# Kernel tuning notes

Measured on AMD Instinct MI355X. Metric: run time of the kernel, lower is better.

The kernel has to match this reference:

```python
import jax, jax.numpy as jnp
import numpy as np

B, T, D, H, KH, HD, F, L, V = 2, 2048, 1024, 16, 4, 64, 4096, 4, 32000
G = H // KH  # num_key_value_groups
EPS = 1e-6
SCALE = HD ** -0.5


def setup_inputs() -> dict:
    key = jax.random.key(0)
    ks = jax.random.split(key, 8)
    std = 0.02
    return {
        "input_ids": jax.random.randint(ks[0], (B, T), 0, V, dtype=jnp.int32),
        "embed_w": jax.random.normal(ks[1], (V, D), jnp.float32) * std,
        "pos_w": jax.random.normal(ks[2], (T, D), jnp.float32) * std,
        "ln1_w": jnp.ones((L, D), jnp.float32),
        "ln2_w": jnp.ones((L, D), jnp.float32),
        "wq": jax.random.normal(ks[3], (L, D, H * HD), jnp.float32) * std,
        "wkv": jax.random.normal(ks[4], (L, D, 2 * KH * HD), jnp.float32) * std,
        "wo": jax.random.normal(ks[5], (L, H * HD, D), jnp.float32) * std,
        "w1": jax.random.normal(ks[6], (L, D, F), jnp.float32) * std,
        "w2": jax.random.normal(ks[7], (L, F, D), jnp.float32) * std,
        "norm_w": jnp.ones((D,), jnp.float32),
    }


def _rmsnorm(x, w):
    return x * jax.lax.rsqrt(jnp.mean(x * x, axis=-1, keepdims=True) + EPS) * w


def reference(input_ids, embed_w, pos_w, ln1_w, ln2_w, wq, wkv, wo, w1, w2, norm_w):
    causal = jnp.tril(jnp.ones((T, T), dtype=bool))  # True = keep
    x = embed_w[input_ids] + pos_w[:T]  # [B,T,D]
    for l in range(L):
        h = _rmsnorm(x, ln1_w[l])
        q = (h @ wq[l]).reshape(B, T, H, HD)
        kv = h @ wkv[l]
        k, v = jnp.split(kv, 2, axis=-1)
        k = jnp.repeat(k.reshape(B, T, KH, HD), G, axis=2)  # GQA repeat_interleave
        v = jnp.repeat(v.reshape(B, T, KH, HD), G, axis=2)
        scores = jnp.einsum("bqhd,bkhd->bhqk", q, k) * SCALE
        scores = jnp.where(causal, scores, -jnp.inf)
        p = jax.nn.softmax(scores, axis=-1)
        o = jnp.einsum("bhqk,bkhd->bqhd", p, v).reshape(B, T, H * HD)
        x = x + o @ wo[l]
        h = _rmsnorm(x, ln2_w[l])
        x = x + jax.nn.gelu(h @ w1[l], approximate=False) @ w2[l]
    x = _rmsnorm(x, norm_w)
    logits = x @ embed_w.T  # tied lm_head
    return logits
```

## Files before the change

kernel.cpp:

```cpp
#include <hip/hip_runtime.h>
#include <hip/hip_bf16.h>

#define DI __device__ __forceinline__

typedef unsigned short u16;
typedef unsigned int u32;
typedef __attribute__((ext_vector_type(8))) short bf16x8;
typedef __attribute__((ext_vector_type(4))) short bf16x4;
typedef __attribute__((ext_vector_type(4))) float f32x4;

#define B_   2
#define T_   2048
#define D_   1024
#define H_   16
#define KH_  4
#define HD_  64
#define F_   4096
#define L_   4
#define V_   32000
#define M_   (B_ * T_)
#define QKVN (H_*HD_ + 2*KH_*HD_)

DI u16 f2bf(float f) {
  __hip_bfloat16 h = __float2bfloat16(f);
  return *reinterpret_cast<u16*>(&h);
}

DI float bf2f(u16 b) {
  __hip_bfloat16 h = *reinterpret_cast<__hip_bfloat16*>(&b);
  return __bfloat162float(h);
}

DI void gl_lds16(const void* g, void* l) {
  __builtin_amdgcn_global_load_lds(
      (const __attribute__((address_space(1))) u32*)g,
      (__attribute__((address_space(3))) u32*)l, 16, 0, 0);
}

#define BARRIER() do { asm volatile("" ::: "memory"); __builtin_amdgcn_s_barrier(); asm volatile("" ::: "memory"); } while (0)
#define LGK0()    asm volatile("s_waitcnt lgkmcnt(0)" ::: "memory")
#define VMC(n)    asm volatile("s_waitcnt vmcnt(" #n ")" ::: "memory")
#define PRIO(p)   __builtin_amdgcn_s_setprio(p)

__global__ __launch_bounds__(256) void embed_kernel(const int* __restrict__ ids,
                                                    const float* __restrict__ ew,
                                                    const float* __restrict__ pw,
                                                    float* __restrict__ x) {
  const int row = blockIdx.x;
  const int t = row & (T_ - 1);
  const int id = ids[row];
  float4 e = reinterpret_cast<const float4*>(ew + (size_t)id * D_)[threadIdx.x];
  float4 p = reinterpret_cast<const float4*>(pw + (size_t)t * D_)[threadIdx.x];
  e.x += p.x; e.y += p.y; e.z += p.z; e.w += p.w;
  reinterpret_cast<float4*>(x + (size_t)row * D_)[threadIdx.x] = e;
}

__global__ __launch_bounds__(256) void conv_kernel(const float* __restrict__ W,
                                                   u16* __restrict__ Wb) {
  const size_t i = (size_t)blockIdx.x * 256 + threadIdx.x;
  float4 v = reinterpret_cast<const float4*>(W)[i];
  ushort4 ov;
  ov.x = f2bf(v.x); ov.y = f2bf(v.y); ov.z = f2bf(v.z); ov.w = f2bf(v.w);
  reinterpret_cast<ushort4*>(Wb)[i] = ov;
}

__global__ __launch_bounds__(256) void convt_fused(const float* __restrict__ wq,
                                                   const float* __restrict__ wkv,
                                                   const float* __restrict__ wo,
                                                   const float* __restrict__ w1,
                                                   const float* __restrict__ w2,
                                                   u16* __restrict__ wtq,
                                                   u16* __restrict__ wto,
                                                   u16* __restrict__ wt1,
                                                   u16* __restrict__ wt2) {
  const int t = blockIdx.x;
  const float* W; u16* Wt; int K, N, local;
  if (t < 1024)      { W = wq;  Wt = wtq;               K = 1024; N = 1024; local = t; }
  else if (t < 1536) { W = wkv; Wt = wtq + 1024*1024;   K = 1024; N = 512;  local = t - 1024; }
  else if (t < 2560) { W = wo;  Wt = wto;               K = 1024; N = 1024; local = t - 1536; }
  else if (t < 6656) { W = w1;  Wt = wt1;               K = 1024; N = 4096; local = t - 2560; }
  else               { W = w2;  Wt = wt2;               K = 4096; N = 1024; local = t - 6656; }
  const int nk = K >> 5;
  const int k0 = (local % nk) * 32, n0 = (local / nk) * 32;
  __shared__ float tb[32][33];
  const int tx = threadIdx.x & 31, ty = threadIdx.x >> 5;
  #pragma unroll
  for (int i = 0; i < 4; i++)
    tb[ty + i*8][tx] = W[(size_t)(k0 + ty + i*8) * N + n0 + tx];
  __syncthreads();
  #pragma unroll
  for (int i = 0; i < 4; i++)
    Wt[(size_t)(n0 + ty + i*8) * K + k0 + tx] = f2bf(tb[tx][ty + i*8]);
}

__global__ __launch_bounds__(256) void rmsnorm_kernel(const float* __restrict__ x,
                                                      const float* __restrict__ w,
                                                      u16* __restrict__ out) {
  const int row = blockIdx.x;
  const int tid = threadIdx.x;
  float4 v = reinterpret_cast<const float4*>(x + (size_t)row * D_)[tid];
  float ss = v.x*v.x + v.y*v.y + v.z*v.z + v.w*v.w;
  #pragma unroll
  for (int off = 32; off > 0; off >>= 1) ss += __shfl_down(ss, off, 64);
  __shared__ float red[4];
  if ((tid & 63) == 0) red[tid >> 6] = ss;
  __syncthreads();
  const float tot = red[0] + red[1] + red[2] + red[3];
  const float rstd = rsqrtf(tot * (1.0f / D_) + 1e-6f);
  float4 wv = reinterpret_cast<const float4*>(w)[tid];
  ushort4 ov;
  ov.x = f2bf(v.x * rstd * wv.x);
  ov.y = f2bf(v.y * rstd * wv.y);
  ov.z = f2bf(v.z * rstd * wv.z);
  ov.w = f2bf(v.w * rstd * wv.w);
  reinterpret_cast<ushort4*>(out + (size_t)row * D_)[tid] = ov;
}

template <int EPI>
__global__ __launch_bounds__(256) void gemm_bt(const u16* __restrict__ A,
                                               const u16* __restrict__ Bt,
                                               const float* __restrict__ res,
                                               u16* __restrict__ Cb,
                                               float* __restrict__ Cf,
                                               int M, int N, int K) {
  __shared__ u16 As[128 * 64];
  __shared__ u16 Bs[128 * 64];
  const int tid = threadIdx.x;
  const int nx = N >> 7;
  const int nwg = nx * (M >> 7);
  const int cpx = nwg >> 3;
  const int bid = blockIdx.x;
  const int wg = (bid & 7) * cpx + (bid >> 3);
  const int n0 = (wg % nx) << 7;
  const int m0 = (wg / nx) << 7;
  const int lane = tid & 63, wave = tid >> 6;
  const int wm = wave >> 1, wn = wave & 1;
  const int l15 = lane & 15, l4 = lane >> 4;
  const int srow = tid >> 3, scol = (tid & 7) * 8;
  const u16* ag = A + (size_t)(m0 + srow) * K + scol;
  const u16* bg = Bt + (size_t)(n0 + srow) * K + scol;
  u16* asd = &As[srow * 64 + scol];
  u16* bsd = &Bs[srow * 64 + scol];
  f32x4 acc[4][4] = {};
  const int nk = K >> 6;
  for (int kt = 0; kt < nk; kt++) {
    const int k0 = kt * 64;
    __syncthreads();
    #pragma unroll
    for (int i = 0; i < 4; i++) gl_lds16(ag + (size_t)i*32*K + k0, asd + i*32*64);
    #pragma unroll
    for (int i = 0; i < 4; i++) gl_lds16(bg + (size_t)i*32*K + k0, bsd + i*32*64);
    __syncthreads();
    #pragma unroll
    for (int s = 0; s < 2; s++) {
      bf16x8 af[4], bfv[4];
      #pragma unroll
      for (int i = 0; i < 4; i++)
        af[i] = *reinterpret_cast<const bf16x8*>(&As[(wm*64 + i*16 + l15)*64 + s*32 + l4*8]);
      #pragma unroll
      for (int j = 0; j < 4; j++)
        bfv[j] = *reinterpret_cast<const bf16x8*>(&Bs[(wn*64 + j*16 + l15)*64 + s*32 + l4*8]);
      #pragma unroll
      for (int i = 0; i < 4; i++)
        #pragma unroll
        for (int j = 0; j < 4; j++)
          acc[i][j] = __builtin_amdgcn_mfma_f32_16x16x32_bf16(bfv[j], af[i], acc[i][j], 0, 0, 0);
    }
  }
  #pragma unroll
  for (int i = 0; i < 4; i++) {
    const int row = m0 + wm*64 + i*16 + l15;
    #pragma unroll
    for (int j = 0; j < 4; j++) {
      const int colb = n0 + wn*64 + j*16 + l4*4;
      const size_t idx = (size_t)row * N + colb;
      const f32x4 v = acc[i][j];
      if (EPI == 0) {
        ushort4 ov;
        ov.x = f2bf(v[0]); ov.y = f2bf(v[1]); ov.z = f2bf(v[2]); ov.w = f2bf(v[3]);
        *reinterpret_cast<ushort4*>(&Cb[idx]) = ov;
      } else {
        const float4 rv = *reinterpret_cast<const float4*>(&res[idx]);
        float4 ov;
        ov.x = v[0] + rv.x; ov.y = v[1] + rv.y; ov.z = v[2] + rv.z; ov.w = v[3] + rv.w;
        *reinterpret_cast<float4*>(&Cf[idx]) = ov;
      }
    }
  }
}

template <int EPI>
__global__ __launch_bounds__(512, 2) void gemm256(const u16* __restrict__ A,
                                                  const u16* __restrict__ Bt,
                                                  u16* __restrict__ Cb,
                                                  float* __restrict__ Cf,
                                                  int M, int N, int K) {
  __shared__ char lds[131072];
  char* const AsB = lds;
  char* const BsB = lds + 65536;
  const int tid = threadIdx.x;
  const int lane = tid & 63, wave = tid >> 6;
  const int wm = wave >> 2, wn = wave & 3;
  const int l15 = lane & 15, l4 = lane >> 4;

  const int nm = M >> 8;
  const int nwg = nm * (N >> 8);
  const int cpx = nwg >> 3;
  const int bid = blockIdx.x;
  const int wg = (bid & 7) * cpx + (bid >> 3);
  const int m0 = (wg % nm) << 8;
  const int n0 = (wg / nm) << 8;

  const u16* const Atile = A + (size_t)m0 * K;
  const u16* const Btile = Bt + (size_t)n0 * K;

  int soff[2][2], pd[2][2];
  #pragma unroll
  for (int h = 0; h < 2; ++h)
    #pragma unroll
    for (int jj = 0; jj < 2; ++jj) {
      const int row = h*128 + jj*64 + (tid >> 3);
      const int sl  = (tid & 7) ^ (row & 7);
      soff[h][jj] = row * K + sl * 8;
      pd[h][jj]   = h*16384 + jj*8192 + tid*16;
    }
  const int swz = (l15 & 7) << 4;
  const int rb0 = l15*128 + ((l4*16)      ^ swz);
  const int rb1 = l15*128 + ((64 + l4*16) ^ swz);

  #define STA(S,H,T) do { const u16* g_ = Atile + (T)*64; char* d_ = AsB + (S)*32768; \
      gl_lds16(g_ + soff[H][0], d_ + pd[H][0]); gl_lds16(g_ + soff[H][1], d_ + pd[H][1]); } while (0)
  #define STB(S,H,T) do { const u16* g_ = Btile + (T)*64; char* d_ = BsB + (S)*32768; \
      gl_lds16(g_ + soff[H][0], d_ + pd[H][0]); gl_lds16(g_ + soff[H][1], d_ + pd[H][1]); } while (0)
  #define RDA(S,GI,RB) (*reinterpret_cast<const bf16x8*>(AsB + (S)*32768 + (GI)*2048 + (RB)))
  #define RDB(S,GJ,RB) (*reinterpret_cast<const bf16x8*>(BsB + (S)*32768 + (GJ)*2048 + (RB)))

  f32x4 acc[8][4] = {};
  bf16x8 Ar[4][2], Br[4][2];

  #define RDA03(S) { _Pragma("unroll") for (int i=0;i<4;++i){ Ar[i][0]=RDA(S,i*2+wm,rb0); Ar[i][1]=RDA(S,i*2+wm,rb1);} }
  #define RDA47(S) { _Pragma("unroll") for (int i=0;i<4;++i){ Ar[i][0]=RDA(S,(i+4)*2+wm,rb0); Ar[i][1]=RDA(S,(i+4)*2+wm,rb1);} }
  #define RDB01(S) { _Pragma("unroll") for (int j=0;j<2;++j){ Br[j][0]=RDB(S,j*4+wn,rb0); Br[j][1]=RDB(S,j*4+wn,rb1);} }
  #define RDB23(S) { _Pragma("unroll") for (int j=2;j<4;++j){ Br[j][0]=RDB(S,j*4+wn,rb0); Br[j][1]=RDB(S,j*4+wn,rb1);} }
  #define MFQ(IO,JL) { _Pragma("unroll") for (int i=0;i<4;++i) _Pragma("unroll") for (int jj=0;jj<2;++jj) { \
      acc[(IO)+i][(JL)+jj] = __builtin_amdgcn_mfma_f32_16x16x32_bf16(Br[(JL)+jj][0], Ar[i][0], acc[(IO)+i][(JL)+jj],0,0,0); \
      acc[(IO)+i][(JL)+jj] = __builtin_amdgcn_mfma_f32_16x16x32_bf16(Br[(JL)+jj][1], Ar[i][1], acc[(IO)+i][(JL)+jj],0,0,0); } }

  STA(0,0,0); STA(0,1,0); STB(0,0,0); STB(0,1,0);
  VMC(4);
  STA(1,0,1); STB(1,0,1); STB(1,1,1);
  VMC(6);
  BARRIER();

  const int niter = K >> 7;
  for (int it = 0; it < niter; ++it) {
    const int t0 = it*2, t1 = t0 + 1;
    const bool pf = (it + 1 < niter);
    RDA03(0); RDB01(0); STA(1,1,t1);
    BARRIER(); LGK0(); PRIO(1); MFQ(0,0); PRIO(0); BARRIER();
    RDB23(0); if (pf) STA(0,0,t0+2);
    BARRIER(); LGK0(); PRIO(1); MFQ(0,2); PRIO(0); BARRIER();
    RDA47(0); if (pf) STB(0,0,t0+2);
    BARRIER(); LGK0(); PRIO(1); MFQ(4,0); PRIO(0); BARRIER();
    if (pf) { STB(0,1,t0+2); VMC(6); } else { VMC(0); }
    BARRIER(); PRIO(1); MFQ(4,2); PRIO(0); BARRIER();
    RDA03(1); RDB01(1); if (pf) STA(0,1,t0+2);
    BARRIER(); LGK0(); PRIO(1); MFQ(0,0); PRIO(0); BARRIER();
    RDB23(1); if (pf) STA(1,0,t1+2);
    BARRIER(); LGK0(); PRIO(1); MFQ(0,2); PRIO(0); BARRIER();
    RDA47(1); if (pf) STB(1,0,t1+2);
    BARRIER(); LGK0(); PRIO(1); MFQ(4,0); PRIO(0); BARRIER();
    if (pf) { STB(1,1,t1+2); VMC(6); }
    BARRIER(); PRIO(1); MFQ(4,2); PRIO(0); BARRIER();
  }

  #pragma unroll
  for (int i = 0; i < 8; ++i) {
    const int row = m0 + (i*2 + wm)*16 + l15;
    #pragma unroll
    for (int j = 0; j < 4; ++j) {
      const int colb = n0 + (j*4 + wn)*16 + l4*4;
      const f32x4 v = acc[i][j];
      if (EPI == 0) {
        *reinterpret_cast<f32x4*>(&Cf[(size_t)row * N + colb]) = v;
      } else {
        ushort4 ov;
        #pragma unroll
        for (int rr = 0; rr < 4; ++rr) {
          const float g = 0.5f * v[rr] * (1.0f + erff(v[rr] * 0.70710678118f));
          ((u16*)&ov)[rr] = f2bf(g);
        }
        *reinterpret_cast<ushort4*>(&Cb[(size_t)row * N + colb]) = ov;
      }
    }
  }
  #undef STA
  #undef STB
  #undef RDA
  #undef RDB
  #undef RDA03
  #undef RDA47
  #undef RDB01
  #undef RDB23
  #undef MFQ
}

__global__ __launch_bounds__(512) void attn_kernel(const u16* __restrict__ qkv,
                                                   u16* __restrict__ o) {
  const int qtA = blockIdx.x;
  const int qtB = 15 - qtA;
  const int h  = blockIdx.y;
  const int b  = blockIdx.z;
  const int kh = h / (H_ / KH_);
  __shared__ u16 Ks[2][64 * 64];
  __shared__ u16 Vt[2][64 * 66];
  __shared__ u16 Pl[16][16 * 68];
  const int tid = threadIdx.x, lane = tid & 63, wave = tid >> 6;
  const int l15 = lane & 15, l4 = lane >> 4;
  const size_t Mrow = (size_t)b * T_;

  bf16x8 qfA[2], qfB[2];
  {
    const u16* qpA = qkv + (Mrow + qtA*128 + wave*16 + l15) * QKVN + h*HD_ + l4*8;
    const u16* qpB = qkv + (Mrow + qtB*128 + wave*16 + l15) * QKVN + h*HD_ + l4*8;
    qfA[0] = *reinterpret_cast<const bf16x8*>(qpA);
    qfA[1] = *reinterpret_cast<const bf16x8*>(qpA + 32);
    qfB[0] = *reinterpret_cast<const bf16x8*>(qpB);
    qfB[1] = *reinterpret_cast<const bf16x8*>(qpB + 32);
    #pragma unroll
    for (int s = 0; s < 2; s++)
      #pragma unroll
      for (int j = 0; j < 8; j++) {
        qfA[s][j] = (short)f2bf(bf2f((u16)qfA[s][j]) * 0.18033688f);
        qfB[s][j] = (short)f2bf(bf2f((u16)qfB[s][j]) * 0.18033688f);
      }
  }
  float mA = -1e30f, lA = 0.0f, mB = -1e30f, lB = 0.0f;
  f32x4 oaccA[4] = {}, oaccB[4] = {};

  const int srow = tid >> 3, scol = (tid & 7) * 8;
  const int vp = (tid >> 4) * 2;
  const int vd = (tid & 15) * 4;
  const u16* const kbase = qkv + Mrow * QKVN + D_ + kh*HD_;
  const u16* const vbase = kbase + KH_*HD_;

  {
    gl_lds16(kbase + (size_t)srow * QKVN + scol, &Ks[0][srow*64 + scol]);
    const u16* vg = vbase + (size_t)vp * QKVN + vd;
    bf16x4 v0 = *reinterpret_cast<const bf16x4*>(vg);
    bf16x4 v1 = *reinterpret_cast<const bf16x4*>(vg + QKVN);
    #pragma unroll
    for (int j = 0; j < 4; j++) {
      const u32 pk = (u32)(u16)v0[j] | ((u32)(u16)v1[j] << 16);
      *reinterpret_cast<u32*>(&Vt[0][(vd + j)*66 + vp]) = pk;
    }
  }
  __syncthreads();

  const int nktA = 2*qtA + 2;
  const int nktB = 2*qtB + 2;
  for (int kt = 0; kt < nktB; kt++) {
    const int cur = kt & 1;
    const bool pf = kt + 1 < nktB;
    bf16x4 v0n, v1n;
    if (pf) {
      gl_lds16(kbase + (size_t)((kt+1)*64 + srow) * QKVN + scol,
               &Ks[1-cur][srow*64 + scol]);
      const u16* vg = vbase + (size_t)((kt+1)*64 + vp) * QKVN + vd;
      v0n = *reinterpret_cast<const bf16x4*>(vg);
      v1n = *reinterpret_cast<const bf16x4*>(vg + QKVN);
    }

    f32x4 saB[4] = {};
    #pragma unroll
    for (int s = 0; s < 2; s++)
      #pragma unroll
      for (int n = 0; n < 4; n++) {
        bf16x8 kf = *reinterpret_cast<const bf16x8*>(&Ks[cur][(n*16 + l15)*64 + s*32 + l4*8]);
        saB[n] = __builtin_amdgcn_mfma_f32_16x16x32_bf16(kf, qfB[s], saB[n], 0, 0, 0);
      }
    if (kt >= 2*qtB) {
      const int qloc = wave*16 + l15;
      const int kb = kt*64 - qtB*128 + l4*4;
      #pragma unroll
      for (int n = 0; n < 4; n++)
        #pragma unroll
        for (int r = 0; r < 4; r++)
          if (kb + n*16 + r > qloc) saB[n][r] = -1e30f;
    }
    {
      float mx;
      {
        f32x4 m4;
        #pragma unroll
        for (int r = 0; r < 4; r++)
          m4[r] = fmaxf(fmaxf(saB[0][r], saB[1][r]), fmaxf(saB[2][r], saB[3][r]));
        mx = fmaxf(fmaxf(m4[0], m4[1]), fmaxf(m4[2], m4[3]));
        mx = fmaxf(mx, __shfl_xor(mx, 16, 64));
        mx = fmaxf(mx, __shfl_xor(mx, 32, 64));
      }
      if (__any((int)(mx - mB > 8.0f))) {
        const float nm = fmaxf(mB, mx);
        const float alpha = exp2f(mB - nm);
        mB = nm; lB *= alpha;
        #pragma unroll
        for (int r = 0; r < 4; r++) {
          const float a_r = __shfl(alpha, l4*4 + r, 64);
          #pragma unroll
          for (int n = 0; n < 4; n++) oaccB[n][r] *= a_r;
        }
      }
      float rs = 0.0f;
      u16* pw = &Pl[8 + wave][0];
      #pragma unroll
      for (int n = 0; n < 4; n++) {
        ushort4 pv;
        #pragma unroll
        for (int r = 0; r < 4; r++) {
          const float p = exp2f(saB[n][r] - mB);
          rs += p;
          ((u16*)&pv)[r] = f2bf(p);
        }
        *reinterpret_cast<ushort4*>(&pw[l15*68 + n*16 + l4*4]) = pv;
      }
      rs += __shfl_xor(rs, 16, 64);
      rs += __shfl_xor(rs, 32, 64);
      lB += rs;
    }

    if (pf) {
      #pragma unroll
      for (int j = 0; j < 4; j++) {
        const u32 pk = (u32)(u16)v0n[j] | ((u32)(u16)v1n[j] << 16);
        *reinterpret_cast<u32*>(&Vt[1-cur][(vd + j)*66 + vp]) = pk;
      }
    }

    asm volatile("s_waitcnt lgkmcnt(0)" ::: "memory");
    #pragma unroll
    for (int s = 0; s < 2; s++) {
      bf16x8 pa = *reinterpret_cast<const bf16x8*>(&Pl[8 + wave][l15*68 + s*32 + l4*8]);
      #pragma unroll
      for (int n = 0; n < 4; n++) {
        bf16x8 vb = *reinterpret_cast<const bf16x8*>(&Vt[cur][(n*16 + l15)*66 + s*32 + l4*8]);
        oaccB[n] = __builtin_amdgcn_mfma_f32_16x16x32_bf16(pa, vb, oaccB[n], 0, 0, 0);
      }
    }

    if (kt < nktA) {
      f32x4 sa[4] = {};
      #pragma unroll
      for (int s = 0; s < 2; s++)
        #pragma unroll
        for (int n = 0; n < 4; n++) {
          bf16x8 kf = *reinterpret_cast<const bf16x8*>(&Ks[cur][(n*16 + l15)*64 + s*32 + l4*8]);
          sa[n] = __builtin_amdgcn_mfma_f32_16x16x32_bf16(kf, qfA[s], sa[n], 0, 0, 0);
        }
      if (kt >= 2*qtA) {
        const int qloc = wave*16 + l15;
        const int kb = kt*64 - qtA*128 + l4*4;
        #pragma unroll
        for (int n = 0; n < 4; n++)
          #pragma unroll
          for (int r = 0; r < 4; r++)
            if (kb + n*16 + r > qloc) sa[n][r] = -1e30f;
      }
      float mx;
      {
        f32x4 m4;
        #pragma unroll
        for (int r = 0; r < 4; r++)
          m4[r] = fmaxf(fmaxf(sa[0][r], sa[1][r]), fmaxf(sa[2][r], sa[3][r]));
        mx = fmaxf(fmaxf(m4[0], m4[1]), fmaxf(m4[2], m4[3]));
        mx = fmaxf(mx, __shfl_xor(mx, 16, 64));
        mx = fmaxf(mx, __shfl_xor(mx, 32, 64));
      }
      if (__any((int)(mx - mA > 8.0f))) {
        const float nm = fmaxf(mA, mx);
        const float alpha = exp2f(mA - nm);
        mA = nm; lA *= alpha;
        #pragma unroll
        for (int r = 0; r < 4; r++) {
          const float a_r = __shfl(alpha, l4*4 + r, 64);
          #pragma unroll
          for (int n = 0; n < 4; n++) oaccA[n][r] *= a_r;
        }
      }
      float rs = 0.0f;
      u16* pw = &Pl[wave][0];
      #pragma unroll
      for (int n = 0; n < 4; n++) {
        ushort4 pv;
        #pragma unroll
        for (int r = 0; r < 4; r++) {
          const float p = exp2f(sa[n][r] - mA);
          rs += p;
          ((u16*)&pv)[r] = f2bf(p);
        }
        *reinterpret_cast<ushort4*>(&pw[l15*68 + n*16 + l4*4]) = pv;
      }
      rs += __shfl_xor(rs, 16, 64);
      rs += __shfl_xor(rs, 32, 64);
      lA += rs;
      asm volatile("s_waitcnt lgkmcnt(0)" ::: "memory");
      #pragma unroll
      for (int s = 0; s < 2; s++) {
        bf16x8 pa = *reinterpret_cast<const bf16x8*>(&pw[l15*68 + s*32 + l4*8]);
        #pragma unroll
        for (int n = 0; n < 4; n++) {
          bf16x8 vb = *reinterpret_cast<const bf16x8*>(&Vt[cur][(n*16 + l15)*66 + s*32 + l4*8]);
          oaccA[n] = __builtin_amdgcn_mfma_f32_16x16x32_bf16(pa, vb, oaccA[n], 0, 0, 0);
        }
      }
    }

    __syncthreads();
  }
  {
    float lr[4];
    #pragma unroll
    for (int r = 0; r < 4; r++) lr[r] = __shfl(lA, l4*4 + r, 64);
    #pragma unroll
    for (int n = 0; n < 4; n++)
      #pragma unroll
      for (int r = 0; r < 4; r++) {
        const float ov = oaccA[n][r] / lr[r];
        const size_t row = Mrow + qtA*128 + wave*16 + l4*4 + r;
        o[row * (size_t)(H_*HD_) + h*HD_ + n*16 + l15] = f2bf(ov);
      }
    #pragma unroll
    for (int r = 0; r < 4; r++) lr[r] = __shfl(lB, l4*4 + r, 64);
    #pragma unroll
    for (int n = 0; n < 4; n++)
      #pragma unroll
      for (int r = 0; r < 4; r++) {
        const float ov = oaccB[n][r] / lr[r];
        const size_t row = Mrow + qtB*128 + wave*16 + l4*4 + r;
        o[row * (size_t)(H_*HD_) + h*HD_ + n*16 + l15] = f2bf(ov);
      }
  }
}

#define OFF_X     0ull
#define OFF_H     16777216ull
#define OFF_QKV   25165824ull
#define OFF_O     37748736ull
#define OFF_U     46137344ull
#define OFF_WTQ   79691776ull
#define OFF_WTO   82837504ull
#define OFF_WT1   84934656ull
#define OFF_WT2   93323264ull
#define OFF_EBF   101711872ull

extern "C" void kernel_launch(void* const* d_in, const int* in_sizes, int n_in,
                              void* d_out, int out_size, void* d_ws, size_t ws_size,
                              hipStream_t stream) {
  const int*   ids = (const int*)  d_in[0];
  const float* ew  = (const float*)d_in[1];
  const float* pw  = (const float*)d_in[2];
  const float* ln1 = (const float*)d_in[3];
  const float* ln2 = (const float*)d_in[4];
  const float* wq  = (const float*)d_in[5];
  const float* wkv = (const float*)d_in[6];
  const float* wo  = (const float*)d_in[7];
  const float* w1  = (const float*)d_in[8];
  const float* w2  = (const float*)d_in[9];
  const float* nw  = (const float*)d_in[10];
  float* out = (float*)d_out;

  char* ws = (char*)d_ws;
  float* x   = (float*)(ws + OFF_X);
  u16*   h   = (u16*)  (ws + OFF_H);
  u16*   qkv = (u16*)  (ws + OFF_QKV);
  u16*   o   = (u16*)  (ws + OFF_O);
  u16*   u   = (u16*)  (ws + OFF_U);
  u16*   wtq = (u16*)  (ws + OFF_WTQ);
  u16*   wto = (u16*)  (ws + OFF_WTO);
  u16*   wt1 = (u16*)  (ws + OFF_WT1);
  u16*   wt2 = (u16*)  (ws + OFF_WT2);
  u16*   ebf = (u16*)  (ws + OFF_EBF);

  embed_kernel<<<M_, 256, 0, stream>>>(ids, ew, pw, x);
  conv_kernel<<<(V_*D_/4)/256, 256, 0, stream>>>(ew, ebf);

  for (int l = 0; l < L_; l++) {
    convt_fused<<<10752, 256, 0, stream>>>(
        wq  + (size_t)l*D_*(H_*HD_),
        wkv + (size_t)l*D_*(2*KH_*HD_),
        wo  + (size_t)l*(H_*HD_)*D_,
        w1  + (size_t)l*D_*F_,
        w2  + (size_t)l*F_*D_,
        wtq, wto, wt1, wt2);

    rmsnorm_kernel<<<M_, 256, 0, stream>>>(x, ln1 + (size_t)l*D_, h);
    gemm_bt<0><<<(QKVN/128)*(M_/128), 256, 0, stream>>>(h, wtq, nullptr, qkv, nullptr, M_, QKVN, D_);
    attn_kernel<<<dim3(T_/256, H_, B_), 512, 0, stream>>>(qkv, o);
    gemm_bt<1><<<(D_/128)*(M_/128), 256, 0, stream>>>(o, wto, x, nullptr, x, M_, D_, H_*HD_);
    rmsnorm_kernel<<<M_, 256, 0, stream>>>(x, ln2 + (size_t)l*D_, h);
    gemm256<1><<<dim3((F_/256)*(M_/256)), 512, 0, stream>>>(h, wt1, u, nullptr, M_, F_, D_);
    gemm_bt<1><<<(D_/128)*(M_/128), 256, 0, stream>>>(u, wt2, x, nullptr, x, M_, D_, F_);
  }

  rmsnorm_kernel<<<M_, 256, 0, stream>>>(x, nw, h);
  gemm256<0><<<dim3((V_/256)*(M_/256)), 512, 0, stream>>>(h, ebf, nullptr, out, M_, V_, D_);
}
```

Baseline: 1.475 ms.

## Make 256-tile GEMM persistent and prefetch next tile during current tile's tail

Converts the 256x256 GEMM into a persistent kernel launched with 256 workgroups, each looping over output tiles with a stride of 256. During the last K-step of the current tile it issues the global-to-LDS loads for the next tile's first K-slices, so that load latency overlaps the final MFMAs and the epilogue. K is hardcoded to 1024. The code assumes consecutive tiles of a workgroup share the same A rows, which holds because the tile stride is a multiple of the 16 M-tiles. The FFN up-projection has exactly 256 tiles, so it gains little; the main target is the LM-head GEMM.

Result: no change. 1.499 ms (+1.7%).

```diff
diff --git a/kernel.cpp b/kernel.cpp
--- a/kernel.cpp
+++ b/kernel.cpp
@@ -190,11 +190,12 @@
 }
 
 template <int EPI>
-__global__ __launch_bounds__(512, 2) void gemm256(const u16* __restrict__ A,
-                                                  const u16* __restrict__ Bt,
-                                                  u16* __restrict__ Cb,
-                                                  float* __restrict__ Cf,
-                                                  int M, int N, int K) {
+__global__ __launch_bounds__(512, 2) void gemm256p(const u16* __restrict__ A,
+                                                   const u16* __restrict__ Bt,
+                                                   u16* __restrict__ Cb,
+                                                   float* __restrict__ Cf,
+                                                   int M, int N) {
+  const int K = 1024;
   __shared__ char lds[131072];
   char* const AsB = lds;
   char* const BsB = lds + 65536;
@@ -204,15 +205,9 @@
   const int l15 = lane & 15, l4 = lane >> 4;
 
   const int nm = M >> 8;
-  const int nwg = nm * (N >> 8);
-  const int cpx = nwg >> 3;
+  const int nt_all = nm * (N >> 8);
   const int bid = blockIdx.x;
-  const int wg = (bid & 7) * cpx + (bid >> 3);
-  const int m0 = (wg % nm) << 8;
-  const int n0 = (wg / nm) << 8;
-
-  const u16* const Atile = A + (size_t)m0 * K;
-  const u16* const Btile = Bt + (size_t)n0 * K;
+  const int wg0 = (bid & 7) * 32 + (bid >> 3);
 
   int soff[2][2], pd[2][2];
   #pragma unroll
@@ -228,9 +223,9 @@
   const int rb0 = l15*128 + ((l4*16)      ^ swz);
   const int rb1 = l15*128 + ((64 + l4*16) ^ swz);
 
-  #define STA(S,H,T) do { const u16* g_ = Atile + (T)*64; char* d_ = AsB + (S)*32768; \
+  #define STA(P,S,H,T) do { const u16* g_ = (P) + (T)*64; char* d_ = AsB + (S)*32768; \
       gl_lds16(g_ + soff[H][0], d_ + pd[H][0]); gl_lds16(g_ + soff[H][1], d_ + pd[H][1]); } while (0)
-  #define STB(S,H,T) do { const u16* g_ = Btile + (T)*64; char* d_ = BsB + (S)*32768; \
+  #define STB(P,S,H,T) do { const u16* g_ = (P) + (T)*64; char* d_ = BsB + (S)*32768; \
       gl_lds16(g_ + soff[H][0], d_ + pd[H][0]); gl_lds16(g_ + soff[H][1], d_ + pd[H][1]); } while (0)
   #define RDA(S,GI,RB) (*reinterpret_cast<const bf16x8*>(AsB + (S)*32768 + (GI)*2048 + (RB)))
   #define RDB(S,GJ,RB) (*reinterpret_cast<const bf16x8*>(BsB + (S)*32768 + (GJ)*2048 + (RB)))
@@ -246,53 +241,84 @@
       acc[(IO)+i][(JL)+jj] = __builtin_amdgcn_mfma_f32_16x16x32_bf16(Br[(JL)+jj][0], Ar[i][0], acc[(IO)+i][(JL)+jj],0,0,0); \
       acc[(IO)+i][(JL)+jj] = __builtin_amdgcn_mfma_f32_16x16x32_bf16(Br[(JL)+jj][1], Ar[i][1], acc[(IO)+i][(JL)+jj],0,0,0); } }
 
-  STA(0,0,0); STA(0,1,0); STB(0,0,0); STB(0,1,0);
+  int tt = wg0;
+  const u16* Ac = A + (size_t)((tt % nm) << 8) * K;
+  const u16* Bc = Bt + (size_t)((tt / nm) << 8) * K;
+
+  STA(Ac,0,0,0); STA(Ac,0,1,0); STB(Bc,0,0,0); STB(Bc,0,1,0);
   VMC(4);
-  STA(1,0,1); STB(1,0,1); STB(1,1,1);
+  STA(Ac,1,0,1); STB(Bc,1,0,1); STB(Bc,1,1,1);
   VMC(6);
   BARRIER();
 
-  const int niter = K >> 7;
-  for (int it = 0; it < niter; ++it) {
-    const int t0 = it*2, t1 = t0 + 1;
-    const bool pf = (it + 1 < niter);
-    RDA03(0); RDB01(0); STA(1,1,t1);
-    BARRIER(); LGK0(); PRIO(1); MFQ(0,0); PRIO(0); BARRIER();
-    RDB23(0); if (pf) STA(0,0,t0+2);
-    BARRIER(); LGK0(); PRIO(1); MFQ(0,2); PRIO(0); BARRIER();
-    RDA47(0); if (pf) STB(0,0,t0+2);
-    BARRIER(); LGK0(); PRIO(1); MFQ(4,0); PRIO(0); BARRIER();
-    if (pf) { STB(0,1,t0+2); VMC(6); } else { VMC(0); }
-    BARRIER(); PRIO(1); MFQ(4,2); PRIO(0); BARRIER();
-    RDA03(1); RDB01(1); if (pf) STA(0,1,t0+2);
-    BARRIER(); LGK0(); PRIO(1); MFQ(0,0); PRIO(0); BARRIER();
-    RDB23(1); if (pf) STA(1,0,t1+2);
-    BARRIER(); LGK0(); PRIO(1); MFQ(0,2); PRIO(0); BARRIER();
-    RDA47(1); if (pf) STB(1,0,t1+2);
-    BARRIER(); LGK0(); PRIO(1); MFQ(4,0); PRIO(0); BARRIER();
-    if (pf) { STB(1,1,t1+2); VMC(6); }
-    BARRIER(); PRIO(1); MFQ(4,2); PRIO(0); BARRIER();
-  }
-
-  #pragma unroll
-  for (int i = 0; i < 8; ++i) {
-    const int row = m0 + (i*2 + wm)*16 + l15;
-    #pragma unroll
-    for (int j = 0; j < 4; ++j) {
-      const int colb = n0 + (j*4 + wn)*16 + l4*4;
-      const f32x4 v = acc[i][j];
-      if (EPI == 0) {
-        *reinterpret_cast<f32x4*>(&Cf[(size_t)row * N + colb]) = v;
-      } else {
-        ushort4 ov;
-        #pragma unroll
-        for (int rr = 0; rr < 4; ++rr) {
-          const float g = 0.5f * v[rr] * (1.0f + erff(v[rr] * 0.70710678118f));
-          ((u16*)&ov)[rr] = f2bf(g);
+  while (tt < nt_all) {
+    const int tn = tt + 256;
+    const bool last = (tn >= nt_all);
+    const u16* An = Ac;
+    const u16* Bn = last ? Bc : (Bt + (size_t)((tn / nm) << 8) * K);
+    for (int it = 0; it < 7; ++it) {
+      const int t0 = it*2, t1 = t0 + 1;
+      RDA03(0); RDB01(0); STA(Ac,1,1,t1);
+      BARRIER(); LGK0(); PRIO(1); MFQ(0,0); PRIO(0); BARRIER();
+      RDB23(0); STA(Ac,0,0,t0+2);
+      BARRIER(); LGK0(); PRIO(1); MFQ(0,2); PRIO(0); BARRIER();
+      RDA47(0); STB(Bc,0,0,t0+2);
+      BARRIER(); LGK0(); PRIO(1); MFQ(4,0); PRIO(0); BARRIER();
+      STB(Bc,0,1,t0+2); VMC(6);
+      BARRIER(); PRIO(1); MFQ(4,2); PRIO(0); BARRIER();
+      RDA03(1); RDB01(1); STA(Ac,0,1,t0+2);
+      BARRIER(); LGK0(); PRIO(1); MFQ(0,0); PRIO(0); BARRIER();
+      RDB23(1); STA(Ac,1,0,t1+2);
+      BARRIER(); LGK0(); PRIO(1); MFQ(0,2); PRIO(0); BARRIER();
+      RDA47(1); STB(Bc,1,0,t1+2);
+      BARRIER(); LGK0(); PRIO(1); MFQ(4,0); PRIO(0); BARRIER();
+      STB(Bc,1,1,t1+2); VMC(6);
+      BARRIER(); PRIO(1); MFQ(4,2); PRIO(0); BARRIER();
+    }
+    {
+      RDA03(0); RDB01(0); STA(Ac,1,1,15);
+      BARRIER(); LGK0(); PRIO(1); MFQ(0,0); PRIO(0); BARRIER();
+      RDB23(0); if (!last) STA(An,0,0,0);
+      BARRIER(); LGK0(); PRIO(1); MFQ(0,2); PRIO(0); BARRIER();
+      RDA47(0); if (!last) STB(Bn,0,0,0);
+      BARRIER(); LGK0(); PRIO(1); MFQ(4,0); PRIO(0); BARRIER();
+      if (!last) { STB(Bn,0,1,0); VMC(6); } else { VMC(0); }
+      BARRIER(); PRIO(1); MFQ(4,2); PRIO(0); BARRIER();
+      RDA03(1); RDB01(1); if (!last) STA(An,0,1,0);
+      BARRIER(); LGK0(); PRIO(1); MFQ(0,0); PRIO(0); BARRIER();
+      RDB23(1); if (!last) STA(An,1,0,1);
+      BARRIER(); LGK0(); PRIO(1); MFQ(0,2); PRIO(0); BARRIER();
+      RDA47(1); if (!last) STB(Bn,1,0,1);
+      BARRIER(); LGK0(); PRIO(1); MFQ(4,0); PRIO(0); BARRIER();
+      if (!last) { STB(Bn,1,1,1); VMC(6); }
+      BARRIER(); PRIO(1); MFQ(4,2); PRIO(0); BARRIER();
+    }
+    {
+      const int m0 = (tt % nm) << 8;
+      const int n0 = (tt / nm) << 8;
+      #pragma unroll
+      for (int i = 0; i < 8; ++i) {
+        const int row = m0 + (i*2 + wm)*16 + l15;
+        #pragma unroll
+        for (int j = 0; j < 4; ++j) {
+          const int colb = n0 + (j*4 + wn)*16 + l4*4;
+          const f32x4 v = acc[i][j];
+          if (EPI == 0) {
+            *reinterpret_cast<f32x4*>(&Cf[(size_t)row * N + colb]) = v;
+          } else {
+            ushort4 ov;
+            #pragma unroll
+            for (int rr = 0; rr < 4; ++rr) {
+              const float g = 0.5f * v[rr] * (1.0f + erff(v[rr] * 0.70710678118f));
+              ((u16*)&ov)[rr] = f2bf(g);
+            }
+            *reinterpret_cast<ushort4*>(&Cb[(size_t)row * N + colb]) = ov;
+          }
+          acc[i][j] = f32x4{0.f, 0.f, 0.f, 0.f};
         }
-        *reinterpret_cast<ushort4*>(&Cb[(size_t)row * N + colb]) = ov;
-      }
-    }
+      }
+    }
+    Ac = An; Bc = Bn; tt = tn;
   }
   #undef STA
   #undef STB
@@ -597,10 +623,10 @@
     attn_kernel<<<dim3(T_/256, H_, B_), 512, 0, stream>>>(qkv, o);
     gemm_bt<1><<<(D_/128)*(M_/128), 256, 0, stream>>>(o, wto, x, nullptr, x, M_, D_, H_*HD_);
     rmsnorm_kernel<<<M_, 256, 0, stream>>>(x, ln2 + (size_t)l*D_, h);
-    gemm256<1><<<dim3((F_/256)*(M_/256)), 512, 0, stream>>>(h, wt1, u, nullptr, M_, F_, D_);
+    gemm256p<1><<<256, 512, 0, stream>>>(h, wt1, u, nullptr, M_, F_);
     gemm_bt<1><<<(D_/128)*(M_/128), 256, 0, stream>>>(u, wt2, x, nullptr, x, M_, D_, F_);
   }
 
   rmsnorm_kernel<<<M_, 256, 0, stream>>>(x, nw, h);
-  gemm256<0><<<dim3((V_/256)*(M_/256)), 512, 0, stream>>>(h, ebf, nullptr, out, M_, V_, D_);
-}
+  gemm256p<0><<<256, 512, 0, stream>>>(h, ebf, nullptr, out, M_, V_);
+}
```
